# Kernel optimization log

Measured on AMD Instinct MI355X. Metric: run time of the kernel, lower is better.

The kernel has to match this reference:

```python
import jax, jax.numpy as jnp
import numpy as np
from jax.scipy.linalg import expm

N, E, HID, L, NH = 128, 64, 256, 4, 8


def _batched_expm(a):
    sh = a.shape
    flat = a.reshape(-1, sh[-2], sh[-1])
    return jax.vmap(expm)(flat).reshape(sh)


def setup_inputs() -> dict:
    key = jax.random.key(0)
    k1, k2, k3, k4 = jax.random.split(key, 4)
    inputs = jax.random.normal(k1, (N, E, HID, L, L), dtype=jnp.float32)
    radial_mask = jax.random.uniform(k2, (N, E), dtype=jnp.float32)
    # torch.nn.Linear default init ~ U(-1/sqrt(fan_in), 1/sqrt(fan_in)); use small normal for stability
    w_in = jax.random.normal(k3, (3 * HID, HID), dtype=jnp.float32) * 0.05
    w_out = jax.random.normal(k4, (HID, HID), dtype=jnp.float32) * 0.05
    rms_norm = jnp.ones((HID,), dtype=jnp.float32)
    return {"inputs": inputs, "radial_mask": radial_mask, "num_heads": NH,
            "w_in": w_in, "w_out": w_out, "rms_norm": rms_norm}


def reference(inputs, radial_mask, num_heads, w_in, w_out, rms_norm):
    n, e, hid, l, _ = inputs.shape
    dh = hid // num_heads

    # custom RMS-style norm: std over channels of the per-channel trace
    trace = jnp.diagonal(inputs, axis1=-2, axis2=-1).sum(-1)          # (n, e, hid)
    std = jnp.std(trace, axis=-1, ddof=1, keepdims=True)[..., None, None]  # (n, e, 1, 1, 1)
    normed = rms_norm[:, None, None] * inputs / (std + 1e-8)         # (n, e, hid, l, l)

    x = normed.transpose(0, 1, 3, 4, 2)                              # (n, e, l, l, hid)
    qkv = jnp.einsum('nelmc,oc->nelmo', x, w_in)                     # (n, e, l, l, 3*hid)
    q, k, v = jnp.split(qkv, 3, axis=-1)

    def to_heads(t):
        t = t.transpose(0, 1, 4, 2, 3)                               # (n, e, hid, l, l)
        t = t.reshape(n, e, num_heads, dh, l, l)
        return t.transpose(0, 2, 1, 3, 4, 5)                         # (n, h, e, dh, l, l)

    q, k, v = to_heads(q), to_heads(k), to_heads(v)

    qk = jnp.einsum('nhelab,nhflbc->nhefac', q, k) / jnp.sqrt(jnp.float32(dh))  # (n,h,e,f,l,l)
    exp = _batched_expm(qk)

    # normalization: trace of sum over f
    denom = jnp.diagonal(exp.sum(axis=-3, keepdims=True), axis1=-2, axis2=-1).sum(-1)  # (n,h,e,1)
    denom = denom[..., None, None]                                   # (n,h,e,1,1,1)
    att = exp * radial_mask[:, None, None, :, None, None] / (denom + 1e-6)

    out = jnp.einsum('nhefab,nhflbc->nhelac', att, v)                # (n,h,e,dh,l,l)
    out = out.transpose(0, 2, 1, 3, 4, 5).reshape(n, e, hid, l, l)
    out = out.transpose(0, 1, 3, 4, 2)                               # (n, e, l, l, hid)
    out = jnp.einsum('nelmc,oc->nelmo', out, w_out)
    out = out.transpose(0, 1, 4, 2, 3)                               # (n, e, hid, l, l)
    return (out + inputs) * jnp.float32(0.5 ** 0.5)
```

## Files before the change

kernel.cpp:

```cpp
#include <hip/hip_runtime.h>
#include <math.h>


#define QKV_SZ   33554432u
#define OF_WINT  0u
#define OF_WOUTT 196608u
#define OF_Q     262144u
#define OF_K     (OF_Q + QKV_SZ)
#define OF_V     (OF_K + QKV_SZ)
#define WS_FLOATS (OF_V + QKV_SZ)

#define QP  20
#define QES 656
#define KP  20
#define KGS 648
#define EE  68
#define EP  276
#define EW  1108

__global__ __launch_bounds__(256) void k_prep(const float* __restrict__ w_in,
                                              const float* __restrict__ w_out,
                                              float* __restrict__ winT,
                                              float* __restrict__ woutT) {
    int idx = blockIdx.x * 256 + threadIdx.x;
    if (idx < 768 * 256) {
        int o = idx >> 8, c = idx & 255;
        winT[c * 768 + o] = w_in[idx];
    }
    if (idx < 256 * 256) {
        int o = idx >> 8, c = idx & 255;
        woutT[c * 256 + o] = w_out[idx];
    }
}

__global__ __launch_bounds__(256, 2) void k_qkv(const float* __restrict__ in,
        const float* __restrict__ winT, const float* __restrict__ rms,
        float* __restrict__ Q, float* __restrict__ Kb, float* __restrict__ Vb) {
    __shared__ __align__(16) float x_l[2][4096];
    __shared__ float red[16];
    int b = blockIdx.x;
    int t = threadIdx.x;
    int w = t >> 6, lane = t & 63;
    const float* src = in + (size_t)(b * 2) * 4096;

    #pragma unroll
    for (int q = 0; q < 4; ++q) {
        *(float4*)(&x_l[0][t*16 + q*4]) = *(const float4*)(src + t*16 + q*4);
        *(float4*)(&x_l[1][t*16 + q*4]) = *(const float4*)(src + 4096 + t*16 + q*4);
    }
    __syncthreads();

    float tr0 = x_l[0][t*16] + x_l[0][t*16+5] + x_l[0][t*16+10] + x_l[0][t*16+15];
    float tr1 = x_l[1][t*16] + x_l[1][t*16+5] + x_l[1][t*16+10] + x_l[1][t*16+15];
    float s0 = tr0, s1 = tr1;
    #pragma unroll
    for (int o = 1; o < 64; o <<= 1) { s0 += __shfl_xor(s0, o); s1 += __shfl_xor(s1, o); }
    if (lane == 0) { red[w] = s0; red[4 + w] = s1; }
    __syncthreads();
    float mean0 = (red[0] + red[1] + red[2] + red[3]) * (1.0f / 256.0f);
    float mean1 = (red[4] + red[5] + red[6] + red[7]) * (1.0f / 256.0f);
    float d0 = tr0 - mean0; d0 *= d0;
    float d1 = tr1 - mean1; d1 *= d1;
    #pragma unroll
    for (int o = 1; o < 64; o <<= 1) { d0 += __shfl_xor(d0, o); d1 += __shfl_xor(d1, o); }
    if (lane == 0) { red[8 + w] = d0; red[12 + w] = d1; }
    __syncthreads();
    float var0 = (red[8] + red[9] + red[10] + red[11]) * (1.0f / 255.0f);
    float var1 = (red[12] + red[13] + red[14] + red[15]) * (1.0f / 255.0f);
    float rv = rms[t];
    float sc0 = rv / (sqrtf(var0) + 1e-8f);
    float sc1 = rv / (sqrtf(var1) + 1e-8f);

    #pragma unroll
    for (int q = 0; q < 4; ++q) {
        float4 v4 = *(float4*)(&x_l[0][t*16 + q*4]);
        v4.x *= sc0; v4.y *= sc0; v4.z *= sc0; v4.w *= sc0;
        *(float4*)(&x_l[0][t*16 + q*4]) = v4;
        float4 u4 = *(float4*)(&x_l[1][t*16 + q*4]);
        u4.x *= sc1; u4.y *= sc1; u4.z *= sc1; u4.w *= sc1;
        *(float4*)(&x_l[1][t*16 + q*4]) = u4;
    }
    __syncthreads();

    int pg = t & 3, og = t >> 2;
    float a0[12][4], a1[12][4];
    #pragma unroll
    for (int j = 0; j < 12; ++j)
        #pragma unroll
        for (int i = 0; i < 4; ++i) { a0[j][i] = 0.f; a1[j][i] = 0.f; }

    const float* wrow = winT + og * 12;
    #pragma unroll 2
    for (int c = 0; c < 256; ++c) {
        float wv[12];
        *(float4*)(wv + 0) = *(const float4*)(wrow + c * 768 + 0);
        *(float4*)(wv + 4) = *(const float4*)(wrow + c * 768 + 4);
        *(float4*)(wv + 8) = *(const float4*)(wrow + c * 768 + 8);
        float4 x0 = *(const float4*)(&x_l[0][c * 16 + pg * 4]);
        float4 x1 = *(const float4*)(&x_l[1][c * 16 + pg * 4]);
        #pragma unroll
        for (int j = 0; j < 12; ++j) {
            float wj = wv[j];
            a0[j][0] += x0.x * wj; a0[j][1] += x0.y * wj;
            a0[j][2] += x0.z * wj; a0[j][3] += x0.w * wj;
            a1[j][0] += x1.x * wj; a1[j][1] += x1.y * wj;
            a1[j][2] += x1.z * wj; a1[j][3] += x1.w * wj;
        }
    }

    #pragma unroll
    for (int si = 0; si < 2; ++si) {
        int site = b * 2 + si;
        int nn = site >> 6, e = site & 63;
        #pragma unroll
        for (int j = 0; j < 12; ++j) {
            int o = og * 12 + j;
            int buf = o >> 8, co = o & 255;
            int h = co >> 5, d = co & 31;
            float* dst = (buf == 0) ? Q : (buf == 1) ? Kb : Vb;
            size_t ad = (((size_t)(nn * 8 + h)) * 64 + e) * 512 + d * 16 + pg * 4;
            const float (*ac)[4] = si ? a1 : a0;
            *(float4*)(dst + ad) = make_float4(ac[j][0], ac[j][1], ac[j][2], ac[j][3]);
        }
    }
}

#define ATTV(P_)                                                              \
    {                                                                         \
        _Pragma("unroll 2")                                                   \
        for (int gg = 0; gg < 4; ++gg) {                                      \
            const float* vb = v_l + gg * KGS + d_o * KP;                      \
            float4 v0 = *(const float4*)(vb + 0);                             \
            float4 v1 = *(const float4*)(vb + 4);                             \
            float4 v2 = *(const float4*)(vb + 8);                             \
            float4 v3 = *(const float4*)(vb + 12);                            \
            _Pragma("unroll")                                                 \
            for (int e2 = 0; e2 < 4; ++e2) {                                  \
                const float* eb = exps_l + w * EW + (P_) * EP + e2 * EE + gg * 16 + half * 8; \
                float4 eA = *(const float4*)(eb + 0);                         \
                float4 eB = *(const float4*)(eb + 4);                         \
                acc[e2][0][0] += eA.x*v0.x + eA.y*v1.x + eA.z*v2.x + eA.w*v3.x; \
                acc[e2][0][1] += eA.x*v0.y + eA.y*v1.y + eA.z*v2.y + eA.w*v3.y; \
                acc[e2][0][2] += eA.x*v0.z + eA.y*v1.z + eA.z*v2.z + eA.w*v3.z; \
                acc[e2][0][3] += eA.x*v0.w + eA.y*v1.w + eA.z*v2.w + eA.w*v3.w; \
                acc[e2][1][0] += eB.x*v0.x + eB.y*v1.x + eB.z*v2.x + eB.w*v3.x; \
                acc[e2][1][1] += eB.x*v0.y + eB.y*v1.y + eB.z*v2.y + eB.w*v3.y; \
                acc[e2][1][2] += eB.x*v0.z + eB.y*v1.z + eB.z*v2.z + eB.w*v3.z; \
                acc[e2][1][3] += eB.x*v0.w + eB.y*v1.w + eB.z*v2.w + eB.w*v3.w; \
            }                                                                 \
        }                                                                     \
    }

#define QK_PHASE(P, MB)                                                       \
    {                                                                         \
        const int fg = s * 4 + (P);                                           \
        __syncthreads();                                                      \
        _Pragma("unroll")                                                     \
        for (int r = 0; r < 2; ++r) {                                         \
            *(float4*)(k_l + sld[r]) = pk[r];                                 \
            if (fg >= 4) *(float4*)(v_l + sld[r]) = pv[r];                    \
        }                                                                     \
        __syncthreads();                                                      \
        if (fg < 15) {                                                        \
            _Pragma("unroll")                                                 \
            for (int r = 0; r < 2; ++r)                                       \
                pk[r] = *(const float4*)(Kg + nhbase + (size_t)(fg + 1) * 2048 + sgo[r]); \
        }                                                                     \
        if (fg >= 3) {                                                        \
            _Pragma("unroll")                                                 \
            for (int r = 0; r < 2; ++r)                                       \
                pv[r] = *(const float4*)(Vg + nhbase + (size_t)(fg - 3) * 2048 + sgo[r]); \
        }                                                                     \
        _Pragma("unroll")                                                     \
        for (int t = 0; t < 16; ++t) MB[t] = 0.f;                             \
        {                                                                     \
            const float* kp = k_l + g * KGS + rep * KP;                       \
            _Pragma("unroll 2")                                               \
            for (int dd = 0; dd < 8; ++dd) {                                  \
                float qa[16], kb[16];                                         \
                const float* qd = qp0 + dd * (4 * QP);                        \
                const float* kd = kp + dd * (4 * KP);                         \
                *(float4*)(qa + 0)  = *(const float4*)(qd + 0);               \
                *(float4*)(qa + 4)  = *(const float4*)(qd + 4);               \
                *(float4*)(qa + 8)  = *(const float4*)(qd + 8);               \
                *(float4*)(qa + 12) = *(const float4*)(qd + 12);              \
                *(float4*)(kb + 0)  = *(const float4*)(kd + 0);               \
                *(float4*)(kb + 4)  = *(const float4*)(kd + 4);               \
                *(float4*)(kb + 8)  = *(const float4*)(kd + 8);               \
                *(float4*)(kb + 12) = *(const float4*)(kd + 12);              \
                _Pragma("unroll")                                             \
                for (int a = 0; a < 4; ++a)                                   \
                    _Pragma("unroll")                                         \
                    for (int bb = 0; bb < 4; ++bb)                            \
                        _Pragma("unroll")                                     \
                        for (int c = 0; c < 4; ++c)                           \
                            MB[a*4+c] += qa[a*4+bb] * kb[bb*4+c];             \
            }                                                                 \
        }                                                                     \
        _Pragma("unroll")                                                     \
        for (int t = 0; t < 16; ++t) {                                        \
            MB[t] += __shfl_xor(MB[t], 16);                                   \
            MB[t] += __shfl_xor(MB[t], 32);                                   \
        }                                                                     \
        if (fg >= 4) ATTV(P);                                                 \
    }

__global__ __launch_bounds__(256, 2) void k_attn(const float* __restrict__ Q,
        const float* __restrict__ Kg, const float* __restrict__ Vg,
        const float* __restrict__ rmask, float* __restrict__ Y) {
    __shared__ __align__(16) float q_l[16 * QES];
    __shared__ __align__(16) float k_l[4 * KGS];
    __shared__ __align__(16) float v_l[4 * KGS];
    __shared__ __align__(16) float exps_l[4 * EW];

    int lb = ((blockIdx.x & 7) << 9) | (blockIdx.x >> 3);
    int eq = lb & 3, h = (lb >> 2) & 7, nn = lb >> 5;
    int tid = threadIdx.x;
    int w = tid >> 6, lane = tid & 63;
    size_t nhbase = ((size_t)(nn * 8 + h)) * (64 * 512);
    int e0 = eq * 16;

    const float rsq = 0.17677669529663687f;

    #pragma unroll
    for (int r = 0; r < 8; ++r) {
        int idx = r * 256 + tid;
        int ee_ = idx >> 7, rem = idx & 127;
        int d = rem >> 2, c4 = rem & 3;
        float4 v4 = *(const float4*)(Q + nhbase + (size_t)(e0 + ee_) * 512 + d * 16 + c4 * 4);
        v4.x *= rsq; v4.y *= rsq; v4.z *= rsq; v4.w *= rsq;
        *(float4*)(q_l + ee_ * QES + d * QP + c4 * 4) = v4;
    }

    int rep = lane >> 4, ee = (lane >> 2) & 3, g = lane & 3;
    int eL = w * 4 + ee;
    int d_o = lane & 31, half = lane >> 5;
    const float* qp0 = q_l + eL * QES + rep * QP;

    int sld[2]; size_t sgo[2];
    #pragma unroll
    for (int r = 0; r < 2; ++r) {
        int slot = r * 256 + tid;
        int gg = slot >> 7, rem = slot & 127;
        int d = rem >> 2, c4 = rem & 3;
        sld[r] = gg * KGS + d * KP + c4 * 4;
        sgo[r] = (size_t)(gg * 512 + d * 16 + c4 * 4);
    }

    float acc[4][2][4];
    #pragma unroll
    for (int a = 0; a < 4; ++a)
        #pragma unroll
        for (int x = 0; x < 2; ++x)
            #pragma unroll
            for (int c = 0; c < 4; ++c) acc[a][x][c] = 0.f;
    float dtr = 0.f;

    float mb0[16], mb1[16], mb2[16], mb3[16];
    float4 pk[2], pv[2];
    #pragma unroll
    for (int r = 0; r < 2; ++r)
        pk[r] = *(const float4*)(Kg + nhbase + sgo[r]);

    #pragma unroll 1
    for (int s = 0; s < 4; ++s) {
        QK_PHASE(0, mb0)
        QK_PHASE(1, mb1)
        QK_PHASE(2, mb2)
        QK_PHASE(3, mb3)

        float mm[16];
        #pragma unroll
        for (int t = 0; t < 16; ++t)
            mm[t] = (rep == 0) ? mb0[t] : (rep == 1) ? mb1[t] : (rep == 2) ? mb2[t] : mb3[t];

        float r0 = fabsf(mm[0])  + fabsf(mm[1])  + fabsf(mm[2])  + fabsf(mm[3]);
        float r1 = fabsf(mm[4])  + fabsf(mm[5])  + fabsf(mm[6])  + fabsf(mm[7]);
        float r2 = fabsf(mm[8])  + fabsf(mm[9])  + fabsf(mm[10]) + fabsf(mm[11]);
        float r3 = fabsf(mm[12]) + fabsf(mm[13]) + fabsf(mm[14]) + fabsf(mm[15]);
        float nrm = fmaxf(fmaxf(r0, r1), fmaxf(r2, r3));
        int sq = 0;
        if (nrm > 0.5f) {
            sq = (int)ceilf(log2f(nrm)) + 1;
            if (sq < 0) sq = 0;
        }
        float sc2 = exp2f((float)(-sq));
        #pragma unroll
        for (int t = 0; t < 16; ++t) mm[t] *= sc2;
        float p[16];
        #pragma unroll
        for (int t = 0; t < 16; ++t) p[t] = 0.f;
        p[0] = p[5] = p[10] = p[15] = 1.f;
        #pragma unroll
        for (int tt = 8; tt >= 1; --tt) {
            float np[16];
            float rr = 1.0f / (float)tt;
            #pragma unroll
            for (int i = 0; i < 4; ++i)
                #pragma unroll
                for (int j = 0; j < 4; ++j) {
                    float s2 = mm[i*4+0]*p[j] + mm[i*4+1]*p[4+j] + mm[i*4+2]*p[8+j] + mm[i*4+3]*p[12+j];
                    np[i*4+j] = ((i == j) ? 1.0f : 0.0f) + s2 * rr;
                }
            #pragma unroll
            for (int t = 0; t < 16; ++t) p[t] = np[t];
        }
        #pragma unroll 1
        for (int it = 0; it < sq; ++it) {
            float np[16];
            #pragma unroll
            for (int i = 0; i < 4; ++i)
                #pragma unroll
                for (int j = 0; j < 4; ++j)
                    np[i*4+j] = p[i*4+0]*p[j] + p[i*4+1]*p[4+j] + p[i*4+2]*p[8+j] + p[i*4+3]*p[12+j];
            #pragma unroll
            for (int t = 0; t < 16; ++t) p[t] = np[t];
        }

        dtr += p[0] + p[5] + p[10] + p[15];

        float mk = rmask[nn * 64 + s * 16 + rep * 4 + g];
        float* eb = exps_l + w * EW + rep * EP + ee * EE + g * 16;
        *(float4*)(eb + 0)  = make_float4(p[0]*mk,  p[1]*mk,  p[2]*mk,  p[3]*mk);
        *(float4*)(eb + 4)  = make_float4(p[4]*mk,  p[5]*mk,  p[6]*mk,  p[7]*mk);
        *(float4*)(eb + 8)  = make_float4(p[8]*mk,  p[9]*mk,  p[10]*mk, p[11]*mk);
        *(float4*)(eb + 12) = make_float4(p[12]*mk, p[13]*mk, p[14]*mk, p[15]*mk);
    }

    #pragma unroll 1
    for (int ep = 0; ep < 4; ++ep) {
        __syncthreads();
        #pragma unroll
        for (int r = 0; r < 2; ++r)
            *(float4*)(v_l + sld[r]) = pv[r];
        __syncthreads();
        if (ep < 3) {
            #pragma unroll
            for (int r = 0; r < 2; ++r)
                pv[r] = *(const float4*)(Vg + nhbase + (size_t)(13 + ep) * 2048 + sgo[r]);
        }
        ATTV(ep)
    }

    dtr += __shfl_xor(dtr, 1);
    dtr += __shfl_xor(dtr, 2);
    dtr += __shfl_xor(dtr, 16);
    dtr += __shfl_xor(dtr, 32);

    #pragma unroll
    for (int e2 = 0; e2 < 4; ++e2) {
        float den = __shfl(dtr, e2 * 4);
        float sO = 1.0f / (den + 1e-6f);
        int e = e0 + w * 4 + e2;
        size_t yb = (((size_t)(nn * 64 + e)) * 256 + h * 32 + d_o) * 16 + half * 8;
        *(float4*)(Y + yb)     = make_float4(acc[e2][0][0]*sO, acc[e2][0][1]*sO, acc[e2][0][2]*sO, acc[e2][0][3]*sO);
        *(float4*)(Y + yb + 4) = make_float4(acc[e2][1][0]*sO, acc[e2][1][1]*sO, acc[e2][1][2]*sO, acc[e2][1][3]*sO);
    }
}

__global__ __launch_bounds__(256, 4) void k_out(const float* __restrict__ Yg,
        const float* __restrict__ woutT, const float* __restrict__ in,
        float* __restrict__ out) {
    __shared__ __align__(16) float y_l[2][4096];
    int b = blockIdx.x;
    int t = threadIdx.x;
    const float* src = Yg + (size_t)(b * 2) * 4096;
    #pragma unroll
    for (int q = 0; q < 4; ++q) {
        *(float4*)(&y_l[0][t*16 + q*4]) = *(const float4*)(src + t*16 + q*4);
        *(float4*)(&y_l[1][t*16 + q*4]) = *(const float4*)(src + 4096 + t*16 + q*4);
    }
    __syncthreads();

    int pg = t & 3, og = t >> 2;
    float a0[4][4], a1[4][4];
    #pragma unroll
    for (int j = 0; j < 4; ++j)
        #pragma unroll
        for (int i = 0; i < 4; ++i) { a0[j][i] = 0.f; a1[j][i] = 0.f; }

    #pragma unroll 2
    for (int c = 0; c < 256; ++c) {
        float4 w4 = *(const float4*)(woutT + c * 256 + og * 4);
        float4 x0 = *(const float4*)(&y_l[0][c * 16 + pg * 4]);
        float4 x1 = *(const float4*)(&y_l[1][c * 16 + pg * 4]);
        a0[0][0] += x0.x*w4.x; a0[0][1] += x0.y*w4.x; a0[0][2] += x0.z*w4.x; a0[0][3] += x0.w*w4.x;
        a0[1][0] += x0.x*w4.y; a0[1][1] += x0.y*w4.y; a0[1][2] += x0.z*w4.y; a0[1][3] += x0.w*w4.y;
        a0[2][0] += x0.x*w4.z; a0[2][1] += x0.y*w4.z; a0[2][2] += x0.z*w4.z; a0[2][3] += x0.w*w4.z;
        a0[3][0] += x0.x*w4.w; a0[3][1] += x0.y*w4.w; a0[3][2] += x0.z*w4.w; a0[3][3] += x0.w*w4.w;
        a1[0][0] += x1.x*w4.x; a1[0][1] += x1.y*w4.x; a1[0][2] += x1.z*w4.x; a1[0][3] += x1.w*w4.x;
        a1[1][0] += x1.x*w4.y; a1[1][1] += x1.y*w4.y; a1[1][2] += x1.z*w4.y; a1[1][3] += x1.w*w4.y;
        a1[2][0] += x1.x*w4.z; a1[2][1] += x1.y*w4.z; a1[2][2] += x1.z*w4.z; a1[2][3] += x1.w*w4.z;
        a1[3][0] += x1.x*w4.w; a1[3][1] += x1.y*w4.w; a1[3][2] += x1.z*w4.w; a1[3][3] += x1.w*w4.w;
    }

    const float RS = 0.70710678118654752f;
    #pragma unroll
    for (int si = 0; si < 2; ++si) {
        const float (*ac)[4] = si ? a1 : a0;
        #pragma unroll
        for (int j = 0; j < 4; ++j) {
            int o = og * 4 + j;
            size_t ad = (size_t)(b * 2 + si) * 4096 + o * 16 + pg * 4;
            float4 i4 = *(const float4*)(in + ad);
            float4 o4;
            o4.x = (ac[j][0] + i4.x) * RS;
            o4.y = (ac[j][1] + i4.y) * RS;
            o4.z = (ac[j][2] + i4.z) * RS;
            o4.w = (ac[j][3] + i4.w) * RS;
            *(float4*)(out + ad) = o4;
        }
    }
}

extern "C" void kernel_launch(void* const* d_in, const int* in_sizes, int n_in,
                              void* d_out, int out_size, void* d_ws, size_t ws_size,
                              hipStream_t stream) {
    const float* inputs = (const float*)d_in[0];
    const float* rmask  = (const float*)d_in[1];
    const float* w_in   = (const float*)d_in[3];
    const float* w_out  = (const float*)d_in[4];
    const float* rms    = (const float*)d_in[5];

    if (ws_size < (size_t)WS_FLOATS * 4ull) return;

    float* ws    = (float*)d_ws;
    float* winT  = ws + OF_WINT;
    float* woutT = ws + OF_WOUTT;
    float* Qb    = ws + OF_Q;
    float* Kb    = ws + OF_K;
    float* Vb    = ws + OF_V;
    float* Y     = (float*)d_out;

    k_prep<<<768,  256, 0, stream>>>(w_in, w_out, winT, woutT);
    k_qkv <<<4096, 256, 0, stream>>>(inputs, winT, rms, Qb, Kb, Vb);
    k_attn<<<4096, 256, 0, stream>>>(Qb, Kb, Vb, rmask, Y);
    k_out <<<4096, 256, 0, stream>>>(Y, woutT, inputs, (float*)d_out);
}
```

Measured before the change: 1.789 ms.

## Double-buffer K/V tiles in LDS and keep scaled Q in registers

Changes the attention kernel so K and V tiles are double-buffered in shared memory. Each phase needs one barrier instead of two, and global prefetch runs two tiles ahead. Q is staged once through shared memory into a per-thread register array (qr[8][16]), and the Q LDS buffer is aliased with the K/V region. This cuts LDS reads and barriers in the QK inner loop, at the cost of roughly 128 extra VGPRs per thread, which may cause spills or lower occupancy under launch_bounds(256,2).

```diff
diff --git a/kernel.cpp b/kernel.cpp
--- a/kernel.cpp
+++ b/kernel.cpp
@@ -10,13 +10,14 @@
 #define OF_V     (OF_K + QKV_SZ)
 #define WS_FLOATS (OF_V + QKV_SZ)
 
-#define QP  20
-#define QES 656
+#define QSE 516
 #define KP  20
 #define KGS 648
+#define KBUF 2592
 #define EE  68
 #define EP  276
 #define EW  1108
+#define SMEMF 14800
 
 __global__ __launch_bounds__(256) void k_prep(const float* __restrict__ w_in,
                                               const float* __restrict__ w_out,
@@ -125,11 +126,12 @@
     }
 }
 
-#define ATTV(P_)                                                              \
+#define ATTV(P_, VBASE)                                                       \
     {                                                                         \
+        const float* vbase_ = (VBASE);                                        \
         _Pragma("unroll 2")                                                   \
         for (int gg = 0; gg < 4; ++gg) {                                      \
-            const float* vb = v_l + gg * KGS + d_o * KP;                      \
+            const float* vb = vbase_ + gg * KGS + d_o * KP;                   \
             float4 v0 = *(const float4*)(vb + 0);                             \
             float4 v1 = *(const float4*)(vb + 4);                             \
             float4 v2 = *(const float4*)(vb + 8);                             \
@@ -151,39 +153,40 @@
         }                                                                     \
     }
 
-#define QK_PHASE(P, MB)                                                       \
+#define PH(P)                                                                 \
     {                                                                         \
         const int fg = s * 4 + (P);                                           \
-        __syncthreads();                                                      \
-        _Pragma("unroll")                                                     \
-        for (int r = 0; r < 2; ++r) {                                         \
-            *(float4*)(k_l + sld[r]) = pk[r];                                 \
-            if (fg >= 4) *(float4*)(v_l + sld[r]) = pv[r];                    \
-        }                                                                     \
+        const int cur = fg & 1;                                               \
         __syncthreads();                                                      \
         if (fg < 15) {                                                        \
             _Pragma("unroll")                                                 \
             for (int r = 0; r < 2; ++r)                                       \
-                pk[r] = *(const float4*)(Kg + nhbase + (size_t)(fg + 1) * 2048 + sgo[r]); \
+                *(float4*)(k_l + (cur^1)*KBUF + sld[r]) = pk[r];              \
         }                                                                     \
         if (fg >= 3) {                                                        \
             _Pragma("unroll")                                                 \
             for (int r = 0; r < 2; ++r)                                       \
-                pv[r] = *(const float4*)(Vg + nhbase + (size_t)(fg - 3) * 2048 + sgo[r]); \
-        }                                                                     \
+                *(float4*)(v_l + (cur^1)*KBUF + sld[r]) = pv[r];              \
+        }                                                                     \
+        if (fg < 14) {                                                        \
+            _Pragma("unroll")                                                 \
+            for (int r = 0; r < 2; ++r)                                       \
+                pk[r] = *(const float4*)(Kg + nhbase + (size_t)(fg + 2) * 2048 + sgo[r]); \
+        }                                                                     \
+        if (fg >= 2) {                                                        \
+            _Pragma("unroll")                                                 \
+            for (int r = 0; r < 2; ++r)                                       \
+                pv[r] = *(const float4*)(Vg + nhbase + (size_t)(fg - 2) * 2048 + sgo[r]); \
+        }                                                                     \
+        float m_[16];                                                         \
         _Pragma("unroll")                                                     \
-        for (int t = 0; t < 16; ++t) MB[t] = 0.f;                             \
+        for (int t = 0; t < 16; ++t) m_[t] = 0.f;                             \
         {                                                                     \
-            const float* kp = k_l + g * KGS + rep * KP;                       \
-            _Pragma("unroll 2")                                               \
+            const float* kp = k_l + cur * KBUF + g * KGS + rep * KP;          \
+            _Pragma("unroll")                                                 \
             for (int dd = 0; dd < 8; ++dd) {                                  \
-                float qa[16], kb[16];                                         \
-                const float* qd = qp0 + dd * (4 * QP);                        \
+                float kb[16];                                                 \
                 const float* kd = kp + dd * (4 * KP);                         \
-                *(float4*)(qa + 0)  = *(const float4*)(qd + 0);               \
-                *(float4*)(qa + 4)  = *(const float4*)(qd + 4);               \
-                *(float4*)(qa + 8)  = *(const float4*)(qd + 8);               \
-                *(float4*)(qa + 12) = *(const float4*)(qd + 12);              \
                 *(float4*)(kb + 0)  = *(const float4*)(kd + 0);               \
                 *(float4*)(kb + 4)  = *(const float4*)(kd + 4);               \
                 *(float4*)(kb + 8)  = *(const float4*)(kd + 8);               \
@@ -194,24 +197,29 @@
                     for (int bb = 0; bb < 4; ++bb)                            \
                         _Pragma("unroll")                                     \
                         for (int c = 0; c < 4; ++c)                           \
-                            MB[a*4+c] += qa[a*4+bb] * kb[bb*4+c];             \
+                            m_[a*4+c] += qr[dd][a*4+bb] * kb[bb*4+c];         \
             }                                                                 \
         }                                                                     \
         _Pragma("unroll")                                                     \
         for (int t = 0; t < 16; ++t) {                                        \
-            MB[t] += __shfl_xor(MB[t], 16);                                   \
-            MB[t] += __shfl_xor(MB[t], 32);                                   \
-        }                                                                     \
-        if (fg >= 4) ATTV(P);                                                 \
+            m_[t] += __shfl_xor(m_[t], 16);                                   \
+            m_[t] += __shfl_xor(m_[t], 32);                                   \
+        }                                                                     \
+        if (rep == (P)) {                                                     \
+            _Pragma("unroll")                                                 \
+            for (int t = 0; t < 16; ++t) mm[t] = m_[t];                       \
+        }                                                                     \
+        if (fg >= 4) ATTV(P, (v_l + cur * KBUF));                             \
     }
 
 __global__ __launch_bounds__(256, 2) void k_attn(const float* __restrict__ Q,
         const float* __restrict__ Kg, const float* __restrict__ Vg,
         const float* __restrict__ rmask, float* __restrict__ Y) {
-    __shared__ __align__(16) float q_l[16 * QES];
-    __shared__ __align__(16) float k_l[4 * KGS];
-    __shared__ __align__(16) float v_l[4 * KGS];
-    __shared__ __align__(16) float exps_l[4 * EW];
+    __shared__ __align__(16) float smem[SMEMF];
+    float* k_l    = smem;
+    float* v_l    = smem + 2 * KBUF;
+    float* exps_l = smem + 4 * KBUF;
+    float* qstage = smem;
 
     int lb = ((blockIdx.x & 7) << 9) | (blockIdx.x >> 3);
     int eq = lb & 3, h = (lb >> 2) & 7, nn = lb >> 5;
@@ -219,8 +227,26 @@
     int w = tid >> 6, lane = tid & 63;
     size_t nhbase = ((size_t)(nn * 8 + h)) * (64 * 512);
     int e0 = eq * 16;
-
     const float rsq = 0.17677669529663687f;
+
+    int rep = lane >> 4, ee = (lane >> 2) & 3, g = lane & 3;
+    int eL = w * 4 + ee;
+    int d_o = lane & 31, half = lane >> 5;
+
+    int sld[2], sgo[2];
+    #pragma unroll
+    for (int r = 0; r < 2; ++r) {
+        int slot = r * 256 + tid;
+        int gg = slot >> 7, rem = slot & 127;
+        int d = rem >> 2, c4 = rem & 3;
+        sld[r] = gg * KGS + d * KP + c4 * 4;
+        sgo[r] = gg * 512 + d * 16 + c4 * 4;
+    }
+
+    float4 pk[2], pv[2];
+    #pragma unroll
+    for (int r = 0; r < 2; ++r)
+        pk[r] = *(const float4*)(Kg + nhbase + sgo[r]);
 
     #pragma unroll
     for (int r = 0; r < 8; ++r) {
@@ -229,23 +255,27 @@
         int d = rem >> 2, c4 = rem & 3;
         float4 v4 = *(const float4*)(Q + nhbase + (size_t)(e0 + ee_) * 512 + d * 16 + c4 * 4);
         v4.x *= rsq; v4.y *= rsq; v4.z *= rsq; v4.w *= rsq;
-        *(float4*)(q_l + ee_ * QES + d * QP + c4 * 4) = v4;
-    }
-
-    int rep = lane >> 4, ee = (lane >> 2) & 3, g = lane & 3;
-    int eL = w * 4 + ee;
-    int d_o = lane & 31, half = lane >> 5;
-    const float* qp0 = q_l + eL * QES + rep * QP;
-
-    int sld[2]; size_t sgo[2];
-    #pragma unroll
-    for (int r = 0; r < 2; ++r) {
-        int slot = r * 256 + tid;
-        int gg = slot >> 7, rem = slot & 127;
-        int d = rem >> 2, c4 = rem & 3;
-        sld[r] = gg * KGS + d * KP + c4 * 4;
-        sgo[r] = (size_t)(gg * 512 + d * 16 + c4 * 4);
-    }
+        *(float4*)(qstage + ee_ * QSE + d * 16 + c4 * 4) = v4;
+    }
+    __syncthreads();
+
+    float qr[8][16];
+    #pragma unroll
+    for (int dd = 0; dd < 8; ++dd) {
+        const float* qs = qstage + eL * QSE + (dd * 4 + rep) * 16;
+        *(float4*)(qr[dd] + 0)  = *(const float4*)(qs + 0);
+        *(float4*)(qr[dd] + 4)  = *(const float4*)(qs + 4);
+        *(float4*)(qr[dd] + 8)  = *(const float4*)(qs + 8);
+        *(float4*)(qr[dd] + 12) = *(const float4*)(qs + 12);
+    }
+    __syncthreads();
+
+    #pragma unroll
+    for (int r = 0; r < 2; ++r)
+        *(float4*)(k_l + sld[r]) = pk[r];
+    #pragma unroll
+    for (int r = 0; r < 2; ++r)
+        pk[r] = *(const float4*)(Kg + nhbase + 2048 + sgo[r]);
 
     float acc[4][2][4];
     #pragma unroll
@@ -255,24 +285,16 @@
             #pragma unroll
             for (int c = 0; c < 4; ++c) acc[a][x][c] = 0.f;
     float dtr = 0.f;
-
-    float mb0[16], mb1[16], mb2[16], mb3[16];
-    float4 pk[2], pv[2];
-    #pragma unroll
-    for (int r = 0; r < 2; ++r)
-        pk[r] = *(const float4*)(Kg + nhbase + sgo[r]);
+    float mm[16];
+    #pragma unroll
+    for (int t = 0; t < 16; ++t) mm[t] = 0.f;
 
     #pragma unroll 1
     for (int s = 0; s < 4; ++s) {
-        QK_PHASE(0, mb0)
-        QK_PHASE(1, mb1)
-        QK_PHASE(2, mb2)
-        QK_PHASE(3, mb3)
-
-        float mm[16];
-        #pragma unroll
-        for (int t = 0; t < 16; ++t)
-            mm[t] = (rep == 0) ? mb0[t] : (rep == 1) ? mb1[t] : (rep == 2) ? mb2[t] : mb3[t];
+        PH(0)
+        PH(1)
+        PH(2)
+        PH(3)
 
         float r0 = fabsf(mm[0])  + fabsf(mm[1])  + fabsf(mm[2])  + fabsf(mm[3]);
         float r1 = fabsf(mm[4])  + fabsf(mm[5])  + fabsf(mm[6])  + fabsf(mm[7]);
@@ -330,16 +352,17 @@
     #pragma unroll 1
     for (int ep = 0; ep < 4; ++ep) {
         __syncthreads();
-        #pragma unroll
-        for (int r = 0; r < 2; ++r)
-            *(float4*)(v_l + sld[r]) = pv[r];
-        __syncthreads();
         if (ep < 3) {
             #pragma unroll
             for (int r = 0; r < 2; ++r)
-                pv[r] = *(const float4*)(Vg + nhbase + (size_t)(13 + ep) * 2048 + sgo[r]);
-        }
-        ATTV(ep)
+                *(float4*)(v_l + ((ep + 1) & 1) * KBUF + sld[r]) = pv[r];
+            if (ep < 2) {
+                #pragma unroll
+                for (int r = 0; r < 2; ++r)
+                    pv[r] = *(const float4*)(Vg + nhbase + (size_t)(14 + ep) * 2048 + sgo[r]);
+            }
+        }
+        ATTV(ep, (v_l + (ep & 1) * KBUF))
     }
 
     dtr += __shfl_xor(dtr, 1);
```

New measurement: 3.306 ms. 84.8% more time.
